# Kernel tuning notes

Measured on AMD Instinct MI355X. Metric: run time of the kernel, lower is better.

## Reference

```python
import jax, jax.numpy as jnp
import numpy as np

EPS = 1e-05

def _rms_norm(x, w, eps=EPS):
    xf = x.astype(jnp.float32)
    var = jnp.mean(xf * xf, axis=-1, keepdims=True)
    return (x * jax.lax.rsqrt(var + eps)) * w

def _apply_rotary_emb(x, freqs_cis):
    # x: [B,S,H,D], freqs_cis: [B,S,D] with cos in first half, sin in second
    half = freqs_cis.shape[-1] // 2
    cos = freqs_cis[..., :half][:, :, None, :]  # [B,S,1,D/2]
    sin = freqs_cis[..., half:][:, :, None, :]
    xf = x.astype(jnp.float32).reshape(*x.shape[:-1], -1, 2)
    xr, xi = xf[..., 0], xf[..., 1]
    out_r = xr * cos - xi * sin
    out_i = xr * sin + xi * cos
    out = jnp.stack([out_r, out_i], axis=-1).reshape(x.shape)
    return out.astype(x.dtype)

def setup_inputs() -> dict:
    key = jax.random.key(0)
    ks = jax.random.split(key, 8)
    B, S, D, H = 2, 4096, 2048, 16
    hd = D // H
    scale = 1.0 / np.sqrt(D)
    x = jax.random.normal(ks[0], (B, S, D), dtype=jnp.float32)
    freqs_cis = jax.random.normal(ks[1], (B, S, hd), dtype=jnp.float32)
    wq = jax.random.normal(ks[2], (D, D), dtype=jnp.float32) * scale
    wk = jax.random.normal(ks[3], (D, D), dtype=jnp.float32) * scale
    wv = jax.random.normal(ks[4], (D, D), dtype=jnp.float32) * scale
    wo = jax.random.normal(ks[5], (D, D), dtype=jnp.float32) * scale
    norm_q_w = jnp.ones((hd,), dtype=jnp.float32)
    norm_k_w = jnp.ones((hd,), dtype=jnp.float32)
    return {"x": x, "freqs_cis": freqs_cis, "wq": wq, "wk": wk, "wv": wv,
            "wo": wo, "norm_q_w": norm_q_w, "norm_k_w": norm_k_w}

def reference(x, freqs_cis, wq, wk, wv, wo, norm_q_w, norm_k_w):
    B, S, D = x.shape
    H = 16
    hd = D // H
    # Linear with torch convention: y = x @ W^T
    q = (x @ wq.T).reshape(B, S, H, hd)
    k = (x @ wk.T).reshape(B, S, H, hd)
    v = (x @ wv.T).reshape(B, S, H, hd)
    q = _rms_norm(q, norm_q_w)
    k = _rms_norm(k, norm_k_w)
    q = _apply_rotary_emb(q, freqs_cis)
    k = _apply_rotary_emb(k, freqs_cis)
    # SDPA: [B,H,S,hd]
    scale = 1.0 / jnp.sqrt(jnp.asarray(hd, dtype=jnp.float32))
    scores = jnp.einsum('bqhd,bkhd->bhqk', q, k) * scale
    attn = jax.nn.softmax(scores, axis=-1)
    out = jnp.einsum('bhqk,bkhd->bqhd', attn, v).reshape(B, S, D)
    return out @ wo.T
```

## Files before the change

kernel.cpp:

```cpp
#include <hip/hip_runtime.h>
#include <hip/hip_bf16.h>
#include <cstdint>
#include <cstdio>

typedef unsigned short ushort_t;
typedef __attribute__((ext_vector_type(8))) __bf16 bf16x8;
typedef __attribute__((ext_vector_type(2))) __bf16 bhalf2_t;
typedef __attribute__((ext_vector_type(8))) unsigned short us8;
typedef __attribute__((ext_vector_type(4))) unsigned short us4;
typedef __attribute__((ext_vector_type(4))) float f32x4;
typedef __attribute__((ext_vector_type(2))) float f32x2;

__device__ __forceinline__ ushort_t f2b(float f) {
  uint32_t u = __builtin_bit_cast(uint32_t, f);
  uint32_t r = (u + 0x7fffu + ((u >> 16) & 1u)) >> 16;
  return (ushort_t)r;
}
__device__ __forceinline__ float b2f(ushort_t s) {
  return __builtin_bit_cast(float, (uint32_t)s << 16);
}

__device__ __forceinline__ void gld_lds16(const void* g, void* l) {
  __builtin_amdgcn_global_load_lds(
      (__attribute__((address_space(1))) void*)(uintptr_t)g,
      (__attribute__((address_space(3))) void*)(uint32_t)(uintptr_t)l,
      16, 0, 0);
}

__global__ void cast_f2b(const float* __restrict__ src, ushort_t* __restrict__ dst, int n4) {
  int i = blockIdx.x * 256 + threadIdx.x;
  if (i < n4) {
    float4 f = ((const float4*)src)[i];
    us4 o = { f2b(f.x), f2b(f.y), f2b(f.z), f2b(f.w) };
    ((us4*)dst)[i] = o;
  }
}

__global__ void cast3_f2b(const float* __restrict__ a, const float* __restrict__ b,
                          const float* __restrict__ c, ushort_t* __restrict__ dst) {
  int i = blockIdx.x * 256 + threadIdx.x;
  int seg = i >> 20, local = i & 1048575;
  const float* src = (seg == 0) ? a : (seg == 1) ? b : c;
  float4 f = ((const float4*)src)[local];
  us4 o = { f2b(f.x), f2b(f.y), f2b(f.z), f2b(f.w) };
  ((us4*)dst)[i] = o;
}

template <typename OutT>
__global__ __launch_bounds__(512, 2) void gemm_bt(const ushort_t* __restrict__ A,
                                                  const ushort_t* __restrict__ B,
                                                  OutT* __restrict__ C,
                                                  int M, int N, int K) {
  __shared__ ushort_t As0[256 * 64], As1[256 * 64];
  __shared__ ushort_t Bs0[256 * 64], Bs1[256 * 64];
  const int w    = threadIdx.x >> 6;
  const int lane = threadIdx.x & 63;
  const int m_l  = lane & 15;
  const int quad = lane >> 4;
  const int m0 = blockIdx.y * 256, n0 = blockIdx.x * 256;
  const int wr = (w >> 2) * 128, wc = (w & 3) * 64;

  f32x4 acc[8][4];
#pragma unroll
  for (int i = 0; i < 8; ++i)
#pragma unroll
    for (int j = 0; j < 4; ++j) acc[i][j] = (f32x4){0.f, 0.f, 0.f, 0.f};

  const int lr = lane >> 3;
  const int sc8 = ((lane & 7) ^ lr) * 8;
  const int ra = w * 32;
  const ushort_t* Ab = A + (size_t)(m0 + ra + lr) * K + sc8;
  const ushort_t* Bb = B + (size_t)(n0 + ra + lr) * K + sc8;

#pragma unroll
  for (int t = 0; t < 4; ++t) {
    gld_lds16(Ab + (size_t)(t * 8) * K, &As0[(ra + t * 8) * 64]);
    gld_lds16(Bb + (size_t)(t * 8) * K, &Bs0[(ra + t * 8) * 64]);
  }
  __syncthreads();

  const int ntile = K >> 6;

  auto tile = [&](const ushort_t* Asc, const ushort_t* Bsc,
                  ushort_t* Asn, ushort_t* Bsn, int ti) {
    if (ti + 1 < ntile) {
      const size_t kn = (size_t)(ti + 1) * 64;
#pragma unroll
      for (int t = 0; t < 4; ++t) {
        gld_lds16(Ab + (size_t)(t * 8) * K + kn, &Asn[(ra + t * 8) * 64]);
        gld_lds16(Bb + (size_t)(t * 8) * K + kn, &Bsn[(ra + t * 8) * 64]);
      }
    }
#pragma unroll
    for (int ph = 0; ph < 4; ++ph) {
      const int mh = ph >> 1, nh = ph & 1;
#pragma unroll
      for (int kk = 0; kk < 2; ++kk) {
        bf16x8 af[4], bg[2];
        const int cx = ((kk * 4 + quad) ^ (m_l & 7)) * 8;
#pragma unroll
        for (int mt = 0; mt < 4; ++mt)
          af[mt] = __builtin_bit_cast(bf16x8,
              *(const us8*)&Asc[(wr + (mh * 4 + mt) * 16 + m_l) * 64 + cx]);
#pragma unroll
        for (int nt = 0; nt < 2; ++nt)
          bg[nt] = __builtin_bit_cast(bf16x8,
              *(const us8*)&Bsc[(wc + (nh * 2 + nt) * 16 + m_l) * 64 + cx]);
        __builtin_amdgcn_s_setprio(1);
#pragma unroll
        for (int mt = 0; mt < 4; ++mt)
#pragma unroll
          for (int nt = 0; nt < 2; ++nt)
            acc[mh * 4 + mt][nh * 2 + nt] = __builtin_amdgcn_mfma_f32_16x16x32_bf16(
                af[mt], bg[nt], acc[mh * 4 + mt][nh * 2 + nt], 0, 0, 0);
        __builtin_amdgcn_s_setprio(0);
      }
    }
    __syncthreads();
  };

  for (int ti = 0; ti < ntile; ti += 2) {
    tile(As0, Bs0, As1, Bs1, ti);
    tile(As1, Bs1, As0, Bs0, ti + 1);
  }

#pragma unroll
  for (int mt = 0; mt < 8; ++mt)
#pragma unroll
    for (int nt = 0; nt < 4; ++nt)
#pragma unroll
      for (int r = 0; r < 4; ++r) {
        int row = m0 + wr + mt * 16 + quad * 4 + r;
        int col = n0 + wc + nt * 16 + m_l;
        float v = acc[mt][nt][r];
        if constexpr (__is_same(OutT, float)) C[(size_t)row * N + col] = v;
        else                                  C[(size_t)row * N + col] = f2b(v);
      }
}

__global__ void rmsrope(ushort_t* __restrict__ qkv, const float* __restrict__ freqs,
                        const float* __restrict__ wq, const float* __restrict__ wk) {
  int w = threadIdx.x >> 6, lane = threadIdx.x & 63;
  int rid = blockIdx.x * 4 + w;
  int h = rid & 15;
  int m = (rid >> 4) & 8191;
  int qk = rid >> 17;
  ushort_t* row = qkv + (size_t)m * 6144 + qk * 2048 + h * 128;
  uint32_t pr = *(const uint32_t*)(row + 2 * lane);
  float xr = b2f((ushort_t)(pr & 0xffff));
  float xi = b2f((ushort_t)(pr >> 16));
  float ss = xr * xr + xi * xi;
#pragma unroll
  for (int o = 1; o < 64; o <<= 1) ss += __shfl_xor(ss, o);
  float rinv = rsqrtf(ss * (1.f / 128.f) + 1e-5f);
  const float* wn = qk ? wk : wq;
  float nr = xr * rinv * wn[2 * lane];
  float ni = xi * rinv * wn[2 * lane + 1];
  float fc = freqs[(size_t)m * 128 + lane];
  float fs = freqs[(size_t)m * 128 + 64 + lane];
  float orr = nr * fc - ni * fs;
  float oii = nr * fs + ni * fc;
  const float k1 = 0.08838834764831845f * 1.4426950408889634f;
  float fscale = (qk == 0) ? k1 : 1.0f;
  orr *= fscale;
  oii *= fscale;
  *(uint32_t*)(row + 2 * lane) = (uint32_t)f2b(orr) | ((uint32_t)f2b(oii) << 16);
}

__global__ void transpose_v(const ushort_t* __restrict__ qkv, ushort_t* __restrict__ vt) {
  __shared__ ushort_t tile[64][136];
  int bh = blockIdx.y, s0 = blockIdx.x * 64;
  int b = bh >> 4, h = bh & 15;
  const ushort_t* src = qkv + (size_t)(b * 4096 + s0) * 6144 + 4096 + h * 128;
  int t = threadIdx.x;
  int r = t >> 2, c0 = (t & 3) * 32;
#pragma unroll
  for (int j = 0; j < 4; ++j)
    *(us8*)&tile[r][c0 + 8 * j] = *(const us8*)(src + (size_t)r * 6144 + c0 + 8 * j);
  __syncthreads();
  int d = t >> 1, sh = (t & 1) * 32;
  ushort_t* dst = vt + (size_t)bh * 524288 + (size_t)d * 4096 + s0 + sh;
#pragma unroll
  for (int i0 = 0; i0 < 32; i0 += 8) {
    us8 o;
#pragma unroll
    for (int j = 0; j < 8; ++j) o[j] = tile[sh + i0 + j][d];
    *(us8*)(dst + i0) = o;
  }
}

__global__ __launch_bounds__(256, 3) void flash_attn(const ushort_t* __restrict__ qkv,
                                                     const ushort_t* __restrict__ vt,
                                                     ushort_t* __restrict__ op0,
                                                     ushort_t* __restrict__ op1,
                                                     ushort_t* __restrict__ op2,
                                                     ushort_t* __restrict__ lbase) {
  __shared__ ushort_t Ks[64 * 128];
  __shared__ ushort_t VTs[128 * 64];

  const int w = threadIdx.x >> 6, lane = threadIdx.x & 63;
  const int m_l = lane & 15, quad = lane >> 4;

  const int id = blockIdx.x;
  const int xcd = id & 7, j = id >> 3;
  const int combo = xcd * 12 + (j >> 5);
  const int q0 = (j & 31) * 128;
  const int bh = combo & 31, split = combo >> 5;
  const int b = bh >> 4, h = bh & 15;
  const int kvbeg = split * 1344;
  const int kvend = (split == 2) ? 4096 : kvbeg + 1344;
  ushort_t* op = (split == 0) ? op0 : (split == 1) ? op1 : op2;

  const ushort_t* qb = qkv + (size_t)(b * 4096 + q0) * 6144 + h * 128;
  const ushort_t* kb = qkv + (size_t)(b * 4096) * 6144 + 2048 + h * 128;
  const ushort_t* vb = vt + (size_t)bh * 524288;

  const int lr = lane >> 4, p15 = lane & 15;

  bf16x8 qf[2][4];
  const int rowq = w * 16 + m_l;
  const int sqr = (m_l & 3) | ((m_l >> 3) << 2) | ((w & 1) << 3);
#pragma unroll
  for (int g = 0; g < 2; ++g) {
    __syncthreads();
#pragma unroll
    for (int t = 0; t < 4; ++t) {
      int rbase = w * 16 + t * 4;
      int sst = lr | ((t >> 1) << 2) | ((w & 1) << 3);
      gld_lds16(qb + (size_t)(g * 64 + rbase + lr) * 6144 + (p15 ^ sst) * 8, &Ks[rbase * 128]);
    }
    __syncthreads();
#pragma unroll
    for (int kk = 0; kk < 4; ++kk)
      qf[g][kk] = __builtin_bit_cast(bf16x8,
          *(const us8*)&Ks[rowq * 128 + ((kk * 4 + quad) ^ sqr) * 8]);
  }

  int kbase[4];
#pragma unroll
  for (int mt = 0; mt < 4; ++mt)
    kbase[mt] = ((m_l >> 2) * 8 + (m_l & 3) + (mt & 1) * 4 + (mt >> 1) * 32) * 128;
  int cx[4];
#pragma unroll
  for (int kk = 0; kk < 4; ++kk) cx[kk] = ((kk * 4 + quad) ^ m_l) * 8;
  int vx[2];
#pragma unroll
  for (int kk = 0; kk < 2; ++kk) vx[kk] = ((kk * 4 + quad) ^ (m_l & 7)) * 8;

  f32x4 lacc[2] = {(f32x4){0.f, 0.f, 0.f, 0.f}, (f32x4){0.f, 0.f, 0.f, 0.f}};
  f32x4 Oa[2][8];
#pragma unroll
  for (int g = 0; g < 2; ++g)
#pragma unroll
    for (int nt = 0; nt < 8; ++nt) Oa[g][nt] = (f32x4){0.f, 0.f, 0.f, 0.f};

  for (int kv0 = kvbeg; kv0 < kvend; kv0 += 64) {
    __syncthreads();
    {
#pragma unroll
      for (int t = 0; t < 4; ++t) {
        int rbase = w * 16 + t * 4;
        int sst = lr | ((t >> 1) << 2) | ((w & 1) << 3);
        gld_lds16(kb + (size_t)(kv0 + rbase + lr) * 6144 + (p15 ^ sst) * 8, &Ks[rbase * 128]);
      }
      int lr2 = lane >> 3, s2 = (lane & 7) ^ lr2;
#pragma unroll
      for (int t = 0; t < 4; ++t) {
        int r = w * 32 + t * 8;
        gld_lds16(vb + (size_t)(r + lr2) * 4096 + kv0 + s2 * 8, &VTs[r * 64]);
      }
    }
    __syncthreads();

    f32x4 S[2][4];
#pragma unroll
    for (int g = 0; g < 2; ++g)
#pragma unroll
      for (int mt = 0; mt < 4; ++mt) S[g][mt] = (f32x4){0.f, 0.f, 0.f, 0.f};
    __builtin_amdgcn_s_setprio(1);
#pragma unroll
    for (int kk = 0; kk < 4; ++kk)
#pragma unroll
      for (int mt = 0; mt < 4; ++mt) {
        bf16x8 kf = __builtin_bit_cast(bf16x8, *(const us8*)&Ks[kbase[mt] + cx[kk]]);
        S[0][mt] = __builtin_amdgcn_mfma_f32_16x16x32_bf16(kf, qf[0][kk], S[0][mt], 0, 0, 0);
        S[1][mt] = __builtin_amdgcn_mfma_f32_16x16x32_bf16(kf, qf[1][kk], S[1][mt], 0, 0, 0);
      }
    __builtin_amdgcn_s_setprio(0);

    union Upf { us8 u; bhalf2_t h[4]; } pf[2][2];
#pragma unroll
    for (int g = 0; g < 2; ++g) {
      f32x4 pe[4];
#pragma unroll
      for (int mt = 0; mt < 4; ++mt)
#pragma unroll
        for (int r = 0; r < 4; ++r)
          pe[mt][r] = __builtin_amdgcn_exp2f(S[g][mt][r]);
      lacc[g] += (pe[0] + pe[1]) + (pe[2] + pe[3]);
#pragma unroll
      for (int kk = 0; kk < 2; ++kk)
#pragma unroll
        for (int t = 0; t < 4; ++t) {
          int mt = kk * 2 + (t >> 1), r0 = (t & 1) * 2;
          f32x2 a = { pe[mt][r0], pe[mt][r0 + 1] };
          pf[g][kk].h[t] = __builtin_convertvector(a, bhalf2_t);
        }
    }

    __builtin_amdgcn_s_setprio(1);
#pragma unroll
    for (int kk = 0; kk < 2; ++kk) {
      bf16x8 p0 = __builtin_bit_cast(bf16x8, pf[0][kk].u);
      bf16x8 p1 = __builtin_bit_cast(bf16x8, pf[1][kk].u);
#pragma unroll
      for (int nt = 0; nt < 8; ++nt) {
        bf16x8 vf = __builtin_bit_cast(bf16x8,
            *(const us8*)&VTs[(nt * 16 + m_l) * 64 + vx[kk]]);
        Oa[0][nt] = __builtin_amdgcn_mfma_f32_16x16x32_bf16(p0, vf, Oa[0][nt], 0, 0, 0);
        Oa[1][nt] = __builtin_amdgcn_mfma_f32_16x16x32_bf16(p1, vf, Oa[1][nt], 0, 0, 0);
      }
    }
    __builtin_amdgcn_s_setprio(0);
  }

#pragma unroll
  for (int g = 0; g < 2; ++g) {
    float lsum = (lacc[g][0] + lacc[g][1]) + (lacc[g][2] + lacc[g][3]);
    lsum += __shfl_xor(lsum, 16);
    lsum += __shfl_xor(lsum, 32);
    if (quad == 0) {
      int s = q0 + g * 64 + w * 16 + m_l;
      *(float*)(lbase + (size_t)(b * 4096 + s) * 6144 + 4096 + h * 128 + split * 2) = lsum;
    }
#pragma unroll
    for (int r = 0; r < 4; ++r) {
      int s = q0 + g * 64 + w * 16 + quad * 4 + r;
      ushort_t* dst = op + (size_t)(b * 4096 + s) * 2048 + h * 128;
#pragma unroll
      for (int nt = 0; nt < 8; ++nt) dst[nt * 16 + m_l] = f2b(Oa[g][nt][r]);
    }
  }
}

__global__ void combine_splits(ushort_t* __restrict__ p0, const ushort_t* __restrict__ p1,
                               const ushort_t* __restrict__ p2, const ushort_t* __restrict__ lbase) {
  int tid = blockIdx.x * 256 + threadIdx.x;
  int row = tid >> 4;
  int brow = row >> 4, h = row & 15;
  const float* lp = (const float*)(lbase + (size_t)brow * 6144 + 4096 + h * 128);
  float inv = 1.f / (lp[0] + lp[1] + lp[2]);
  size_t off = (size_t)tid * 8;
  us8 a = *(const us8*)(p0 + off);
  us8 bb = *(const us8*)(p1 + off);
  us8 c = *(const us8*)(p2 + off);
  us8 o;
#pragma unroll
  for (int i = 0; i < 8; ++i)
    o[i] = f2b((b2f(a[i]) + b2f(bb[i]) + b2f(c[i])) * inv);
  *(us8*)(p0 + off) = o;
}

extern "C" void kernel_launch(void* const* d_in, const int* in_sizes, int n_in,
                              void* d_out, int out_size, void* d_ws, size_t ws_size,
                              hipStream_t stream) {
  const float* x     = (const float*)d_in[0];
  const float* freqs = (const float*)d_in[1];
  const float* wq    = (const float*)d_in[2];
  const float* wk    = (const float*)d_in[3];
  const float* wv    = (const float*)d_in[4];
  const float* wo    = (const float*)d_in[5];
  const float* nqw   = (const float*)d_in[6];
  const float* nkw   = (const float*)d_in[7];
  float* out = (float*)d_out;

  char* ws = (char*)d_ws;
  ushort_t* xb    = (ushort_t*)(ws);
  ushort_t* wqkvb = (ushort_t*)(ws + 33554432);
  ushort_t* qkvb  = (ushort_t*)(ws + 67108864);
  ushort_t* vtb   = (ushort_t*)(ws + 167772160);
  ushort_t* ctxb  = (ushort_t*)(ws + 201326592);
  ushort_t* part2 = wqkvb;
  ushort_t* wob2  = xb;
  if (ws_size < 234881024) { fprintf(stderr, "kernel_launch: ws too small (%zu < 234881024)\n", ws_size); return; }

  cast_f2b<<<16384, 256, 0, stream>>>(x, xb, 4194304);
  cast3_f2b<<<12288, 256, 0, stream>>>(wq, wk, wv, wqkvb);

  gemm_bt<ushort_t><<<dim3(24, 32), 512, 0, stream>>>(xb, wqkvb, qkvb, 8192, 6144, 2048);
  rmsrope<<<65536, 256, 0, stream>>>(qkvb, freqs, nqw, nkw);
  transpose_v<<<dim3(64, 32), 256, 0, stream>>>(qkvb, vtb);
  flash_attn<<<3072, 256, 0, stream>>>(qkvb, vtb, ctxb, xb, part2, qkvb);
  combine_splits<<<8192, 256, 0, stream>>>(ctxb, xb, part2, qkvb);
  cast_f2b<<<4096, 256, 0, stream>>>(wo, wob2, 1048576);
  gemm_bt<float><<<dim3(8, 32), 512, 0, stream>>>(ctxb, wob2, out, 8192, 2048, 2048);
}
```

Measured before the change: 784.6 us.

## Restructure bf16 GEMM pipeline with staggered A/B prefetch and per-phase barriers

Reworks the main GEMM's K-loop so that the B tile for step k+1 is issued in halves interleaved with the MFMA phases, and the A tile is prefetched two steps ahead into the buffer just consumed. Fragment loads for both k-substeps are hoisted ahead of the MFMAs in each phase. Full __syncthreads is replaced with explicit s_waitcnt vmcnt counts and s_barrier. The aim is to hide global-to-LDS latency behind compute and to avoid draining every outstanding load each tile. The cost is more barriers per tile and hand-counted vmcnt values that must stay in step with the number of issued loads.

```diff
diff --git a/kernel.cpp b/kernel.cpp
--- a/kernel.cpp
+++ b/kernel.cpp
@@ -45,6 +45,36 @@
   us4 o = { f2b(f.x), f2b(f.y), f2b(f.z), f2b(f.w) };
   ((us4*)dst)[i] = o;
 }
+
+#define GEMM_PHASE(Asc, Bsc, MH, NH, STAGE)                                          \
+  do {                                                                               \
+    bf16x8 af[2][4], bg[2][2];                                                       \
+    _Pragma("unroll")                                                                \
+    for (int kk = 0; kk < 2; ++kk) {                                                 \
+      const int cx = ((kk * 4 + quad) ^ (m_l & 7)) * 8;                              \
+      _Pragma("unroll")                                                              \
+      for (int mt = 0; mt < 4; ++mt)                                                 \
+        af[kk][mt] = __builtin_bit_cast(bf16x8,                                      \
+            *(const us8*)&Asc[(wr + ((MH) * 4 + mt) * 16 + m_l) * 64 + cx]);         \
+      _Pragma("unroll")                                                              \
+      for (int nt = 0; nt < 2; ++nt)                                                 \
+        bg[kk][nt] = __builtin_bit_cast(bf16x8,                                      \
+            *(const us8*)&Bsc[(wc + ((NH) * 2 + nt) * 16 + m_l) * 64 + cx]);         \
+    }                                                                                \
+    STAGE;                                                                           \
+    __builtin_amdgcn_s_barrier();                                                    \
+    __builtin_amdgcn_s_setprio(1);                                                   \
+    _Pragma("unroll")                                                                \
+    for (int kk = 0; kk < 2; ++kk)                                                   \
+      _Pragma("unroll")                                                              \
+      for (int mt = 0; mt < 4; ++mt)                                                 \
+        _Pragma("unroll")                                                            \
+        for (int nt = 0; nt < 2; ++nt)                                               \
+          acc[(MH) * 4 + mt][(NH) * 2 + nt] = __builtin_amdgcn_mfma_f32_16x16x32_bf16( \
+              af[kk][mt], bg[kk][nt], acc[(MH) * 4 + mt][(NH) * 2 + nt], 0, 0, 0);   \
+    __builtin_amdgcn_s_setprio(0);                                                   \
+    __builtin_amdgcn_s_barrier();                                                    \
+  } while (0)
 
 template <typename OutT>
 __global__ __launch_bounds__(512, 2) void gemm_bt(const ushort_t* __restrict__ A,
@@ -68,60 +98,56 @@
 
   const int lr = lane >> 3;
   const int sc8 = ((lane & 7) ^ lr) * 8;
-  const int ra = w * 32;
-  const ushort_t* Ab = A + (size_t)(m0 + ra + lr) * K + sc8;
-  const ushort_t* Bb = B + (size_t)(n0 + ra + lr) * K + sc8;
-
-#pragma unroll
-  for (int t = 0; t < 4; ++t) {
-    gld_lds16(Ab + (size_t)(t * 8) * K, &As0[(ra + t * 8) * 64]);
-    gld_lds16(Bb + (size_t)(t * 8) * K, &Bs0[(ra + t * 8) * 64]);
-  }
-  __syncthreads();
+  const ushort_t* Abase = A + (size_t)(m0 + lr) * K + sc8;
+  const ushort_t* Bbase = B + (size_t)(n0 + lr) * K + sc8;
+
+  auto stageA = [&](ushort_t* dst, int kt, int h) {
+#pragma unroll
+    for (int t = 0; t < 2; ++t) {
+      const int r0 = h * 128 + w * 16 + t * 8;
+      gld_lds16(Abase + (size_t)r0 * K + (size_t)kt * 64, &dst[r0 * 64]);
+    }
+  };
+  auto stageB = [&](ushort_t* dst, int kt, int h) {
+#pragma unroll
+    for (int t = 0; t < 2; ++t) {
+      const int r0 = h * 128 + w * 16 + t * 8;
+      gld_lds16(Bbase + (size_t)r0 * K + (size_t)kt * 64, &dst[r0 * 64]);
+    }
+  };
 
   const int ntile = K >> 6;
 
-  auto tile = [&](const ushort_t* Asc, const ushort_t* Bsc,
-                  ushort_t* Asn, ushort_t* Bsn, int ti) {
-    if (ti + 1 < ntile) {
-      const size_t kn = (size_t)(ti + 1) * 64;
-#pragma unroll
-      for (int t = 0; t < 4; ++t) {
-        gld_lds16(Ab + (size_t)(t * 8) * K + kn, &Asn[(ra + t * 8) * 64]);
-        gld_lds16(Bb + (size_t)(t * 8) * K + kn, &Bsn[(ra + t * 8) * 64]);
-      }
-    }
-#pragma unroll
-    for (int ph = 0; ph < 4; ++ph) {
-      const int mh = ph >> 1, nh = ph & 1;
-#pragma unroll
-      for (int kk = 0; kk < 2; ++kk) {
-        bf16x8 af[4], bg[2];
-        const int cx = ((kk * 4 + quad) ^ (m_l & 7)) * 8;
-#pragma unroll
-        for (int mt = 0; mt < 4; ++mt)
-          af[mt] = __builtin_bit_cast(bf16x8,
-              *(const us8*)&Asc[(wr + (mh * 4 + mt) * 16 + m_l) * 64 + cx]);
-#pragma unroll
-        for (int nt = 0; nt < 2; ++nt)
-          bg[nt] = __builtin_bit_cast(bf16x8,
-              *(const us8*)&Bsc[(wc + (nh * 2 + nt) * 16 + m_l) * 64 + cx]);
-        __builtin_amdgcn_s_setprio(1);
-#pragma unroll
-        for (int mt = 0; mt < 4; ++mt)
-#pragma unroll
-          for (int nt = 0; nt < 2; ++nt)
-            acc[mh * 4 + mt][nh * 2 + nt] = __builtin_amdgcn_mfma_f32_16x16x32_bf16(
-                af[mt], bg[nt], acc[mh * 4 + mt][nh * 2 + nt], 0, 0, 0);
-        __builtin_amdgcn_s_setprio(0);
-      }
-    }
-    __syncthreads();
+  stageA(As0, 0, 0); stageA(As0, 0, 1);
+  stageB(Bs0, 0, 0); stageB(Bs0, 0, 1);
+  if (ntile > 1) {
+    stageA(As1, 1, 0); stageA(As1, 1, 1);
+    asm volatile("s_waitcnt vmcnt(4)" ::: "memory");
+  } else {
+    asm volatile("s_waitcnt vmcnt(0)" ::: "memory");
+  }
+  __builtin_amdgcn_s_barrier();
+
+  auto tileStep = [&](ushort_t* Asc, ushort_t* Bsc, ushort_t* Asn, ushort_t* Bsn, int ti) {
+    const bool pf = (ti + 1 < ntile);
+    GEMM_PHASE(Asc, Bsc, 0, 0, { if (pf) stageB(Bsn, ti + 1, 0); });
+    GEMM_PHASE(Asc, Bsc, 0, 1, { if (pf) stageB(Bsn, ti + 1, 1); });
+    GEMM_PHASE(Asc, Bsc, 1, 0, {});
+    GEMM_PHASE(Asc, Bsc, 1, 1, {});
+    if (ti + 2 < ntile) {
+      stageA(Asc, ti + 2, 0);
+      stageA(Asc, ti + 2, 1);
+      asm volatile("s_waitcnt vmcnt(4)" ::: "memory");
+      __builtin_amdgcn_s_barrier();
+    } else if (ti + 1 < ntile) {
+      asm volatile("s_waitcnt vmcnt(0)" ::: "memory");
+      __builtin_amdgcn_s_barrier();
+    }
   };
 
   for (int ti = 0; ti < ntile; ti += 2) {
-    tile(As0, Bs0, As1, Bs1, ti);
-    tile(As1, Bs1, As0, Bs0, ti + 1);
+    tileStep(As0, Bs0, As1, Bs1, ti);
+    tileStep(As1, Bs1, As0, Bs0, ti + 1);
   }
 
 #pragma unroll
```

New measurement: 805.3 us. 1.03x slower.
